# Kernel tuning notes

Hardware: AMD Instinct MI355X
Metric: run time of the kernel (lower is better)

Reference implementation:

```python
import jax, jax.numpy as jnp
import numpy as np

N = 20000      # nodes (spots)
D = 256        # embed_dim
H = 4          # n_heads
DH = D // H    # head dim
L = 2          # n_layers
E = 320000     # edges (avg degree 16)
K = 48         # static padded-neighbor cap (>= true max degree for this data)
EPS = 1e-5
NEG = -1e30


def setup_inputs() -> dict:
    key = jax.random.key(0)
    ks = jax.random.split(key, 8)
    s = 0.05
    return {
        "expr_embed": jax.random.normal(ks[0], (N, D), jnp.float32),
        "spatial_embed": jax.random.normal(ks[1], (N, D), jnp.float32),
        "in_proj_w": jax.random.normal(ks[2], (L, 3 * D, D), jnp.float32) * s,
        "in_proj_b": jnp.zeros((L, 3 * D), jnp.float32),
        "out_proj_w": jax.random.normal(ks[3], (L, D, D), jnp.float32) * s,
        "out_proj_b": jnp.zeros((L, D), jnp.float32),
        "ffn_w1": jax.random.normal(ks[4], (L, 2 * D, D), jnp.float32) * s,
        "ffn_b1": jnp.zeros((L, 2 * D), jnp.float32),
        "ffn_w2": jax.random.normal(ks[5], (L, D, 2 * D), jnp.float32) * s,
        "ffn_b2": jnp.zeros((L, D), jnp.float32),
        "ln1_g": jnp.ones((L, D), jnp.float32),
        "ln1_b": jnp.zeros((L, D), jnp.float32),
        "ln2_g": jnp.ones((L, D), jnp.float32),
        "ln2_b": jnp.zeros((L, D), jnp.float32),
        "edge_index": jax.random.randint(ks[6], (2, E), 0, N, jnp.int32),
    }


def _build_neighbors(edge_index):
    """Padded neighbor indices (N,K) and key_padding_mask (N,K) (True = pad)."""
    src, tgt = edge_index[0], edge_index[1]
    counts = jnp.zeros((N,), jnp.int32).at[tgt].add(1)
    order = jnp.argsort(tgt)                       # group edges by target
    src_s, tgt_s = src[order], tgt[order]
    offsets = jnp.concatenate([jnp.zeros((1,), jnp.int32),
                               jnp.cumsum(counts)[:-1].astype(jnp.int32)])
    pos = jnp.arange(E, dtype=jnp.int32) - offsets[tgt_s]
    pos = jnp.where(pos < K, pos, K)               # K is out-of-bounds -> dropped
    nbr = jnp.zeros((N, K), jnp.int32).at[tgt_s, pos].set(src_s, mode='drop')
    pad = jnp.ones((N, K), bool).at[tgt_s, pos].set(False, mode='drop')
    iso = counts == 0                              # isolated spots attend to self
    nbr = nbr.at[:, 0].set(jnp.where(iso, jnp.arange(N, dtype=jnp.int32), nbr[:, 0]))
    pad = pad.at[:, 0].set(jnp.where(iso, False, pad[:, 0]))
    return nbr, pad


def _layernorm(x, g, b):
    mu = jnp.mean(x, -1, keepdims=True)
    var = jnp.var(x, -1, keepdims=True)
    return (x - mu) * jax.lax.rsqrt(var + EPS) * g + b


def _forward(expr_embed, spatial_embed, in_proj_w, in_proj_b, out_proj_w,
             out_proj_b, ffn_w1, ffn_b1, ffn_w2, ffn_b2,
             ln1_g, ln1_b, ln2_g, ln2_b, nbr, pad):
    x = expr_embed
    scale = 1.0 / jnp.sqrt(jnp.asarray(DH, x.dtype))
    for i in range(L):
        Wq, Wk, Wv = jnp.split(in_proj_w[i], 3, axis=0)
        bq, bk, bv = jnp.split(in_proj_b[i], 3, axis=0)
        q = (x @ Wq.T + bq).reshape(N, H, DH)
        # project spatial once, gather projected rows (same math as gather-then-project)
        k = (spatial_embed @ Wk.T + bk)[nbr].reshape(N, K, H, DH)
        v = (spatial_embed @ Wv.T + bv)[nbr].reshape(N, K, H, DH)
        scores = jnp.einsum('nhd,nkhd->nhk', q, k) * scale      # (N,H,K)
        scores = jnp.where(pad[:, None, :], NEG, scores)
        attn = jax.nn.softmax(scores, axis=-1)
        ao = jnp.einsum('nhk,nkhd->nhd', attn, v).reshape(N, D)
        ao = ao @ out_proj_w[i].T + out_proj_b[i]
        x = _layernorm(x + ao, ln1_g[i], ln1_b[i])
        h = jax.nn.gelu(x @ ffn_w1[i].T + ffn_b1[i], approximate=False)
        h = h @ ffn_w2[i].T + ffn_b2[i]
        x = _layernorm(x + h, ln2_g[i], ln2_b[i])
    return x


def reference(expr_embed, spatial_embed, in_proj_w, in_proj_b, out_proj_w,
              out_proj_b, ffn_w1, ffn_b1, ffn_w2, ffn_b2,
              ln1_g, ln1_b, ln2_g, ln2_b, edge_index):
    nbr, pad = _build_neighbors(edge_index.astype(jnp.int32))
    return _forward(expr_embed, spatial_embed, in_proj_w, in_proj_b, out_proj_w,
                    out_proj_b, ffn_w1, ffn_b1, ffn_w2, ffn_b2,
                    ln1_g, ln1_b, ln2_g, ln2_b, nbr, pad)
```

## Files before the change

kernel.cpp:

```cpp
#include <hip/hip_runtime.h>

#define N_NODES 20000
#define DIM 256
#define NHEAD 4
#define DHEAD 64
#define NLAYER 2
#define NEDGE 320000
#define KCAP 48
#define NBM64 313
#define NBM32 625

typedef __bf16 v8bf __attribute__((ext_vector_type(8)));
typedef __bf16 v2bf __attribute__((ext_vector_type(2)));
typedef float v4f __attribute__((ext_vector_type(4)));

union U32 { unsigned u; v2bf v; };

__device__ __forceinline__ unsigned short f2bf(float f) {
    unsigned u = __float_as_uint(f);
    unsigned r = u + 0x7FFFu + ((u >> 16) & 1u);
    return (unsigned short)(r >> 16);
}
__device__ __forceinline__ float bflo(unsigned u) { return __uint_as_float(u << 16); }
__device__ __forceinline__ float bfhi(unsigned u) { return __uint_as_float(u & 0xFFFF0000u); }

__device__ __forceinline__ void gl2lds(const void* g, void* l) {
    __builtin_amdgcn_global_load_lds(
        (const __attribute__((address_space(1))) unsigned int*)g,
        (__attribute__((address_space(3))) unsigned int*)l, 16, 0, 0);
}

__device__ __forceinline__ void stage8(const unsigned short* __restrict__ g0,
                                       size_t stride_e, unsigned short* lds) {
    const int l = threadIdx.x & 63;
    const int r = l >> 3;
    const int c = (l & 7) ^ r;
    gl2lds(g0 + (size_t)r * stride_e + c * 8, lds);
}
__device__ __forceinline__ void stage8c(const unsigned short* __restrict__ base,
                                        int row0, int rowmax, size_t stride_e,
                                        int k0, unsigned short* lds) {
    const int l = threadIdx.x & 63;
    const int r = l >> 3;
    const int c = (l & 7) ^ r;
    int row = row0 + r; row = row > rowmax ? rowmax : row;
    gl2lds(base + (size_t)row * stride_e + k0 + c * 8, lds);
}

__device__ __forceinline__ v8bf frag_read(const unsigned short* lds, int row, int col2) {
    const int bo = row * 128 + (col2 ^ ((row & 7) << 4));
    return *(const v8bf*)((const char*)lds + bo);
}

__global__ void sniffzero_kernel(const unsigned short* __restrict__ p,
                                 int* __restrict__ flag, int* __restrict__ cnt) {
    if (blockIdx.x == 0) {
        __shared__ int s;
        if (threadIdx.x == 0) s = 0;
        __syncthreads();
        int c = 0;
        for (int i = threadIdx.x; i < 4096; i += 256) {
            unsigned short u = p[i];
            unsigned e = (u >> 7) & 0xFFu;
            if (e == 0xFFu) c++;
            else if (e == 0u && (u & 0x7Fu)) c++;
        }
        atomicAdd(&s, c);
        __syncthreads();
        if (threadIdx.x == 0) flag[0] = (s >= 4) ? 1 : 0;
    } else {
        int i = (blockIdx.x - 1) * 256 + threadIdx.x;
        if (i < N_NODES) cnt[i] = 0;
    }
}

struct ConvBfArgs { const void* src[6]; unsigned short* dst[6]; int n[6]; };

__global__ void conv_bf16_kernel(ConvBfArgs a, const int* __restrict__ flag) {
    const int t  = blockIdx.y;
    const int n  = a.n[t];
    const int i0 = (blockIdx.x * 256 + threadIdx.x) * 4;
    if (i0 >= n) return;
    unsigned short* dst = a.dst[t];
    if (flag[0]) {
        float4 v = *(const float4*)((const float*)a.src[t] + i0);
        ushort4 o;
        o.x = f2bf(v.x); o.y = f2bf(v.y); o.z = f2bf(v.z); o.w = f2bf(v.w);
        *(ushort4*)(dst + i0) = o;
    } else {
        ushort4 u = *(const ushort4*)((const unsigned short*)a.src[t] + i0);
        *(ushort4*)(dst + i0) = u;
    }
}

struct ConvF32Args { const void* src[8]; float* dst[8]; int n[8]; };

__global__ void conv_f32_kernel(ConvF32Args a, const int* __restrict__ flag) {
    const int t  = blockIdx.y;
    const int n  = a.n[t];
    const int i0 = (blockIdx.x * 256 + threadIdx.x) * 4;
    if (i0 >= n) return;
    float* dst = a.dst[t];
    if (flag[0]) {
        float4 v = *(const float4*)((const float*)a.src[t] + i0);
        *(float4*)(dst + i0) = v;
    } else {
        ushort4 u = *(const ushort4*)((const unsigned short*)a.src[t] + i0);
        *(float4*)(dst + i0) = make_float4(bflo(u.x), bflo(u.y), bflo(u.z), bflo(u.w));
    }
}

__global__ void build_nbr_kernel(const int* __restrict__ ei,
                                 int* __restrict__ cnt, int* __restrict__ nbr) {
    int e = blockIdx.x * 256 + threadIdx.x;
    if (e >= NEDGE) return;
    int s = ei[e];
    int t = ei[NEDGE + e];
    int slot = atomicAdd(&cnt[t], 1);
    if (slot < KCAP) nbr[t * KCAP + slot] = s;
}

__device__ __forceinline__ void gemm_body64(
    unsigned short* At, unsigned short* Bt,
    const unsigned short* __restrict__ A, const unsigned short* __restrict__ B,
    const float* __restrict__ bias, unsigned short* __restrict__ C,
    int M, int Nc, int Kd, int m0, int nB, int nC, int do_gelu)
{
    const int tid  = threadIdx.x;
    const int wave = tid >> 6;
    const int lane = tid & 63;
    const int wr   = (wave >> 1) * 32;
    const int wc   = (wave & 1) * 64;
    const int lm   = lane & 15;
    const int lk   = (lane >> 4) * 8;

    v4f acc[2][4] = {};

    for (int k0 = 0; k0 < Kd; k0 += 64) {
#pragma unroll
        for (int i = 0; i < 2; ++i) {
            const int rr = wave * 16 + i * 8;
            stage8c(A, m0 + rr, M - 1, Kd, k0, At + rr * 64);
        }
#pragma unroll
        for (int i = 0; i < 4; ++i) {
            const int rr = wave * 32 + i * 8;
            stage8(B + (size_t)(nB + rr) * Kd + k0, Kd, Bt + rr * 64);
        }
        __syncthreads();

#pragma unroll
        for (int ks = 0; ks < 2; ++ks) {
            v8bf af[2], bq[4];
#pragma unroll
            for (int mi = 0; mi < 2; ++mi)
                af[mi] = frag_read(At, wr + mi * 16 + lm, (ks * 32 + lk) * 2);
#pragma unroll
            for (int ni = 0; ni < 4; ++ni)
                bq[ni] = frag_read(Bt, wc + ni * 16 + lm, (ks * 32 + lk) * 2);
#pragma unroll
            for (int mi = 0; mi < 2; ++mi)
#pragma unroll
                for (int ni = 0; ni < 4; ++ni)
                    acc[mi][ni] = __builtin_amdgcn_mfma_f32_16x16x32_bf16(
                        af[mi], bq[ni], acc[mi][ni], 0, 0, 0);
        }
        __syncthreads();
    }

    const int rq = (lane >> 4) << 2;
#pragma unroll
    for (int ni = 0; ni < 4; ++ni) {
        int colb = wc + ni * 16 + lm;
        float bv = bias[nB + colb];
        int colc = nC + colb;
#pragma unroll
        for (int mi = 0; mi < 2; ++mi) {
#pragma unroll
            for (int r = 0; r < 4; ++r) {
                int row = m0 + wr + mi * 16 + rq + r;
                if (row >= M) continue;
                float v = acc[mi][ni][r] + bv;
                if (do_gelu) v = 0.5f * v * (1.0f + erff(v * 0.7071067811865475f));
                C[(size_t)row * Nc + colc] = f2bf(v);
            }
        }
    }
}

__global__ __launch_bounds__(256) void gemm_kernel(
    const unsigned short* __restrict__ A, const unsigned short* __restrict__ B,
    const float* __restrict__ bias, unsigned short* __restrict__ C,
    int M, int Nc, int Kd, int do_gelu)
{
    __shared__ __align__(1024) unsigned short At[64 * 64];
    __shared__ __align__(1024) unsigned short Bt[128 * 64];
    const int n0 = blockIdx.y * 128;
    gemm_body64(At, Bt, A, B, bias, C, M, Nc, Kd, blockIdx.x * 64, n0, n0, do_gelu);
}

__global__ __launch_bounds__(256) void qkv_kernel(
    const unsigned short* __restrict__ x, const unsigned short* __restrict__ spat,
    const unsigned short* __restrict__ W, const float* __restrict__ bias,
    unsigned short* __restrict__ q, unsigned short* __restrict__ kv, int M)
{
    __shared__ __align__(1024) unsigned short At[64 * 64];
    __shared__ __align__(1024) unsigned short Bt[128 * 64];
    const int y = blockIdx.y;
    const unsigned short* A = (y < 2) ? x : spat;
    unsigned short*       C = (y < 2) ? q : kv;
    const int Nc = (y < 2) ? 256 : 512;
    const int nB = y * 128;
    const int nC = (y < 2) ? nB : nB - 256;
    gemm_body64(At, Bt, A, W, bias, C, M, Nc, 256, blockIdx.x * 64, nB, nC, 0);
}

__global__ __launch_bounds__(256) void gemm_ln_kernel(
    const unsigned short* __restrict__ A, const unsigned short* __restrict__ B,
    const float* __restrict__ bias, const unsigned short* __restrict__ xres,
    const float* __restrict__ g, const float* __restrict__ bb,
    unsigned short* __restrict__ xout, void* __restrict__ dout,
    int M, int Kd, int final_out, const int* __restrict__ flag)
{
    __shared__ __align__(1024) unsigned short At[32 * 64];
    __shared__ __align__(1024) unsigned short Bt[256 * 64];
    __shared__ float partS[4][32], partSS[4][32];
    __shared__ float totMu[32], totR[32];

    const int tid  = threadIdx.x;
    const int m0   = blockIdx.x * 32;
    const int wave = tid >> 6;
    const int lane = tid & 63;
    const int wn0  = wave * 64;
    const int lm   = lane & 15;
    const int lk   = (lane >> 4) * 8;

    v4f acc[2][4] = {};

    for (int k0 = 0; k0 < Kd; k0 += 64) {
        {
            const int rr = wave * 8;
            stage8c(A, m0 + rr, M - 1, Kd, k0, At + rr * 64);
        }
#pragma unroll
        for (int i = 0; i < 8; ++i) {
            const int rr = wave * 64 + i * 8;
            stage8(B + (size_t)rr * Kd + k0, Kd, Bt + rr * 64);
        }
        __syncthreads();

#pragma unroll
        for (int ks = 0; ks < 2; ++ks) {
            v8bf af[2], bq[4];
#pragma unroll
            for (int mi = 0; mi < 2; ++mi)
                af[mi] = frag_read(At, mi * 16 + lm, (ks * 32 + lk) * 2);
#pragma unroll
            for (int ni = 0; ni < 4; ++ni)
                bq[ni] = frag_read(Bt, wn0 + ni * 16 + lm, (ks * 32 + lk) * 2);
#pragma unroll
            for (int mi = 0; mi < 2; ++mi)
#pragma unroll
                for (int ni = 0; ni < 4; ++ni)
                    acc[mi][ni] = __builtin_amdgcn_mfma_f32_16x16x32_bf16(
                        af[mi], bq[ni], acc[mi][ni], 0, 0, 0);
        }
        __syncthreads();
    }

    const int rq = (lane >> 4) << 2;
    float gv[4], bv2[4], biasv[4];
#pragma unroll
    for (int ni = 0; ni < 4; ++ni) {
        int col = wn0 + ni * 16 + lm;
        biasv[ni] = bias[col];
        gv[ni]    = g[col];
        bv2[ni]   = bb[col];
    }

    float sl[2][4] = {}, ssl[2][4] = {};
#pragma unroll
    for (int mi = 0; mi < 2; ++mi) {
#pragma unroll
        for (int r = 0; r < 4; ++r) {
            int row = m0 + mi * 16 + rq + r;
#pragma unroll
            for (int ni = 0; ni < 4; ++ni) {
                int col = wn0 + ni * 16 + lm;
                float resv = bflo((unsigned)xres[(size_t)row * DIM + col]);
                float v = acc[mi][ni][r] + biasv[ni] + resv;
                acc[mi][ni][r] = v;
                sl[mi][r]  += v;
                ssl[mi][r] += v * v;
            }
        }
    }
#pragma unroll
    for (int mi = 0; mi < 2; ++mi)
#pragma unroll
        for (int r = 0; r < 4; ++r) {
#pragma unroll
            for (int m = 1; m <= 8; m <<= 1) {
                sl[mi][r]  += __shfl_xor(sl[mi][r],  m, 64);
                ssl[mi][r] += __shfl_xor(ssl[mi][r], m, 64);
            }
        }
    if (lm == 0) {
#pragma unroll
        for (int mi = 0; mi < 2; ++mi)
#pragma unroll
            for (int r = 0; r < 4; ++r) {
                partS[wave][mi * 16 + rq + r]  = sl[mi][r];
                partSS[wave][mi * 16 + rq + r] = ssl[mi][r];
            }
    }
    __syncthreads();
    if (tid < 32) {
        float S = partS[0][tid] + partS[1][tid] + partS[2][tid] + partS[3][tid];
        float SS = partSS[0][tid] + partSS[1][tid] + partSS[2][tid] + partSS[3][tid];
        float mu  = S * (1.0f / DIM);
        float var = SS * (1.0f / DIM) - mu * mu;
        totMu[tid] = mu;
        totR[tid]  = rsqrtf(var + 1e-5f);
    }
    __syncthreads();

#pragma unroll
    for (int mi = 0; mi < 2; ++mi) {
#pragma unroll
        for (int r = 0; r < 4; ++r) {
            int lrow = mi * 16 + rq + r;
            int row  = m0 + lrow;
            float mu = totMu[lrow];
            float rv = totR[lrow];
#pragma unroll
            for (int ni = 0; ni < 4; ++ni) {
                int col = wn0 + ni * 16 + lm;
                float o = (acc[mi][ni][r] - mu) * rv * gv[ni] + bv2[ni];
                if (final_out) {
                    if (flag[0]) ((float*)dout)[(size_t)row * DIM + col] = o;
                    else ((unsigned short*)dout)[(size_t)row * DIM + col] = f2bf(o);
                } else {
                    xout[(size_t)row * DIM + col] = f2bf(o);
                }
            }
        }
    }
}

__global__ __launch_bounds__(256) void attn_kernel(
    const unsigned short* __restrict__ q,
    const unsigned short* __restrict__ kv,
    const int* __restrict__ nbr,
    const int* __restrict__ cnt,
    unsigned short* __restrict__ ao)
{
    const int n    = blockIdx.x;
    const int tid  = threadIdx.x;
    const int h    = tid >> 6;
    const int lane = tid & 63;

    __shared__ float sc[NHEAD][KCAP];
    __shared__ int   nbs[NHEAD][KCAP];

    int deg = cnt[n];
    if (deg > KCAP) deg = KCAP;
    const bool iso = (deg == 0);
    if (iso) deg = 1;

    if (lane < KCAP)
        nbs[h][lane] = (lane < deg) ? (iso ? n : nbr[n * KCAP + lane]) : 0;

    const int sub = lane & 7;
    const int grp = lane >> 3;
    const uint4 qu = *(const uint4*)&q[(size_t)n * DIM + h * DHEAD + sub * 8];
    const unsigned short* kbase = kv + h * DHEAD + sub * 8;
    const int nit = (deg + 7) >> 3;

    const int quarter = lane >> 4;
    const int d0      = (lane & 15) * 4;
    const unsigned short* vbase = kv + 256 + h * DHEAD + d0;
    const int dmax = (deg + 3) & ~3;
    const int npv  = dmax >> 2;

    uint4 ku[6];
#pragma unroll
    for (int it = 0; it < 6; ++it) {
        if (it < nit) {
            int nb = nbs[h][it * 8 + grp];
            ku[it] = *(const uint4*)&kbase[(size_t)nb * 512];
        }
    }
    uint2 vu[8];
#pragma unroll
    for (int it = 0; it < 8; ++it) {
        if (it < npv) {
            int nb = nbs[h][it * 4 + quarter];
            vu[it] = *(const uint2*)&vbase[(size_t)nb * 512];
        }
    }

#pragma unroll
    for (int it = 0; it < 6; ++it) {
        if (it < nit) {
            int j = it * 8 + grp;
            uint4 kz = ku[it];
#if __has_builtin(__builtin_amdgcn_fdot2_f32_bf16)
            U32 a0{qu.x}, a1{qu.y}, a2{qu.z}, a3{qu.w};
            U32 b0{kz.x}, b1{kz.y}, b2{kz.z}, b3{kz.w};
            float p = __builtin_amdgcn_fdot2_f32_bf16(a0.v, b0.v, 0.0f, false);
            p = __builtin_amdgcn_fdot2_f32_bf16(a1.v, b1.v, p, false);
            p = __builtin_amdgcn_fdot2_f32_bf16(a2.v, b2.v, p, false);
            p = __builtin_amdgcn_fdot2_f32_bf16(a3.v, b3.v, p, false);
#else
            float p = bflo(qu.x) * bflo(kz.x);
            p = fmaf(bfhi(qu.x), bfhi(kz.x), p);
            p = fmaf(bflo(qu.y), bflo(kz.y), p);
            p = fmaf(bfhi(qu.y), bfhi(kz.y), p);
            p = fmaf(bflo(qu.z), bflo(kz.z), p);
            p = fmaf(bfhi(qu.z), bfhi(kz.z), p);
            p = fmaf(bflo(qu.w), bflo(kz.w), p);
            p = fmaf(bfhi(qu.w), bfhi(kz.w), p);
#endif
            p += __shfl_xor(p, 1, 64);
            p += __shfl_xor(p, 2, 64);
            p += __shfl_xor(p, 4, 64);
            if (sub == 0 && j < deg) sc[h][j] = p * 0.125f;
        }
    }

    {
        float s  = (lane < deg) ? sc[h][lane] : -1e30f;
        float mx = s;
#pragma unroll
        for (int m = 32; m >= 1; m >>= 1) mx = fmaxf(mx, __shfl_xor(mx, m, 64));
        float e   = (lane < deg) ? __expf(s - mx) : 0.0f;
        float sum = e;
#pragma unroll
        for (int m = 32; m >= 1; m >>= 1) sum += __shfl_xor(sum, m, 64);
        float inv = 1.0f / sum;
        if (lane < KCAP) sc[h][lane] = e * inv;
    }

    {
        float a0 = 0.f, a1 = 0.f, a2 = 0.f, a3 = 0.f;
#pragma unroll
        for (int it = 0; it < 8; ++it) {
            if (it < npv) {
                float w = sc[h][it * 4 + quarter];
                uint2 u = vu[it];
                a0 = fmaf(w, bflo(u.x), a0);
                a1 = fmaf(w, bfhi(u.x), a1);
                a2 = fmaf(w, bflo(u.y), a2);
                a3 = fmaf(w, bfhi(u.y), a3);
            }
        }
        for (int j = 32; j < dmax; j += 4) {
            int j0 = j + quarter;
            int nb = nbs[h][j0];
            uint2 u = *(const uint2*)&vbase[(size_t)nb * 512];
            float w = sc[h][j0];
            a0 = fmaf(w, bflo(u.x), a0);
            a1 = fmaf(w, bfhi(u.x), a1);
            a2 = fmaf(w, bflo(u.y), a2);
            a3 = fmaf(w, bfhi(u.y), a3);
        }
        a0 += __shfl_xor(a0, 16, 64); a0 += __shfl_xor(a0, 32, 64);
        a1 += __shfl_xor(a1, 16, 64); a1 += __shfl_xor(a1, 32, 64);
        a2 += __shfl_xor(a2, 16, 64); a2 += __shfl_xor(a2, 32, 64);
        a3 += __shfl_xor(a3, 16, 64); a3 += __shfl_xor(a3, 32, 64);
        if (lane < 16) {
            uint2 o;
            o.x = (unsigned)f2bf(a0) | ((unsigned)f2bf(a1) << 16);
            o.y = (unsigned)f2bf(a2) | ((unsigned)f2bf(a3) << 16);
            *(uint2*)&ao[(size_t)n * DIM + h * DHEAD + d0] = o;
        }
    }
}

extern "C" void kernel_launch(void* const* d_in, const int* in_sizes, int n_in,
                              void* d_out, int out_size, void* d_ws, size_t ws_size,
                              hipStream_t stream) {
    const int* ei = (const int*)d_in[14];

    char* ws = (char*)d_ws;
    size_t off = 0;
    auto alloc = [&](size_t bytes) -> void* {
        void* p = ws + off;
        off = (off + bytes + 255) & ~(size_t)255;
        return p;
    };

    const int bidx[6] = { 0, 1, 2, 4, 6, 8 };
    const int bnn[6]  = { N_NODES * DIM, N_NODES * DIM,
                          NLAYER * 3 * DIM * DIM, NLAYER * DIM * DIM,
                          NLAYER * 2 * DIM * DIM, NLAYER * DIM * 2 * DIM };
    ConvBfArgs cb;
    unsigned short* canb[6];
    for (int i = 0; i < 6; ++i) {
        canb[i] = (unsigned short*)alloc((size_t)bnn[i] * 2);
        cb.src[i] = d_in[bidx[i]];
        cb.dst[i] = canb[i];
        cb.n[i]   = bnn[i];
    }
    const unsigned short* expr_b = canb[0];
    const unsigned short* spat_b = canb[1];
    const unsigned short* ipw    = canb[2];
    const unsigned short* opw    = canb[3];
    const unsigned short* w1     = canb[4];
    const unsigned short* w2     = canb[5];

    const int fidx[8] = { 3, 5, 7, 9, 10, 11, 12, 13 };
    const int fn[8]   = { NLAYER * 3 * DIM, NLAYER * DIM, NLAYER * 2 * DIM,
                          NLAYER * DIM, NLAYER * DIM, NLAYER * DIM,
                          NLAYER * DIM, NLAYER * DIM };
    ConvF32Args cf;
    float* canf[8];
    for (int i = 0; i < 8; ++i) {
        canf[i] = (float*)alloc((size_t)fn[i] * 4);
        cf.src[i] = d_in[fidx[i]];
        cf.dst[i] = canf[i];
        cf.n[i]   = fn[i];
    }

    unsigned short* x_buf  = (unsigned short*)alloc((size_t)N_NODES * DIM * 2);
    unsigned short* q_buf  = (unsigned short*)alloc((size_t)N_NODES * DIM * 2);
    unsigned short* kv_buf = (unsigned short*)alloc((size_t)N_NODES * 2 * DIM * 2);
    unsigned short* ao_buf = (unsigned short*)alloc((size_t)N_NODES * DIM * 2);
    unsigned short* h_buf  = (unsigned short*)alloc((size_t)N_NODES * 2 * DIM * 2);
    int* cnt  = (int*)alloc((size_t)N_NODES * 4);
    int* nbr  = (int*)alloc((size_t)N_NODES * KCAP * 4);
    int* flag = (int*)alloc(256);

    sniffzero_kernel<<<1 + (N_NODES + 255) / 256, 256, 0, stream>>>(
        (const unsigned short*)d_in[0], flag, cnt);
    conv_bf16_kernel<<<dim3((N_NODES * DIM) / 1024, 6), 256, 0, stream>>>(cb, flag);
    conv_f32_kernel<<<dim3(2, 8), 256, 0, stream>>>(cf, flag);
    build_nbr_kernel<<<(NEDGE + 255) / 256, 256, 0, stream>>>(ei, cnt, nbr);

    for (int i = 0; i < NLAYER; ++i) {
        const unsigned short* Wqkv = ipw + (size_t)i * 3 * DIM * DIM;
        const float*          bqkv = canf[0] + (size_t)i * 3 * DIM;
        const unsigned short* xin  = (i == 0) ? expr_b : x_buf;

        qkv_kernel<<<dim3(NBM64, 6), 256, 0, stream>>>(
            xin, spat_b, Wqkv, bqkv, q_buf, kv_buf, N_NODES);
        attn_kernel<<<N_NODES, 256, 0, stream>>>(q_buf, kv_buf, nbr, cnt, ao_buf);
        gemm_ln_kernel<<<NBM32, 256, 0, stream>>>(
            ao_buf, opw + (size_t)i * DIM * DIM, canf[1] + (size_t)i * DIM,
            xin, canf[4] + (size_t)i * DIM, canf[5] + (size_t)i * DIM,
            x_buf, nullptr, N_NODES, DIM, 0, flag);
        gemm_kernel<<<dim3(NBM64, 4), 256, 0, stream>>>(
            x_buf, w1 + (size_t)i * 2 * DIM * DIM, canf[2] + (size_t)i * 2 * DIM,
            h_buf, N_NODES, 2 * DIM, DIM, 1);
        gemm_ln_kernel<<<NBM32, 256, 0, stream>>>(
            h_buf, w2 + (size_t)i * DIM * 2 * DIM, canf[3] + (size_t)i * DIM,
            x_buf, canf[6] + (size_t)i * DIM, canf[7] + (size_t)i * DIM,
            x_buf, d_out, N_NODES, 2 * DIM, (i == NLAYER - 1) ? 1 : 0, flag);
    }
}
```

Measured before the change: 399.4 us.

## Fuse FFN up-projection, GELU, down-projection and LayerNorm into one kernel

Replaces the separate W1 GEMM (with GELU) and the W2 GEMM+LayerNorm kernels with a single kernel per 32-row tile. The tile streams W1/W2 in 32-column chunks, keeps the GELU hidden activations in LDS, and accumulates the second GEMM in registers before the residual add and LayerNorm. This removes the global round trip of the N×512 hidden buffer and one launch per layer. In exchange, every block re-reads the full W1 and W2 through cache, uses small per-wave MFMA tiles, and needs three barriers per chunk, so the kernel may become latency-bound.

```diff
diff --git a/kernel.cpp b/kernel.cpp
--- a/kernel.cpp
+++ b/kernel.cpp
@@ -49,6 +49,11 @@
 
 __device__ __forceinline__ v8bf frag_read(const unsigned short* lds, int row, int col2) {
     const int bo = row * 128 + (col2 ^ ((row & 7) << 4));
+    return *(const v8bf*)((const char*)lds + bo);
+}
+
+__device__ __forceinline__ v8bf frag32(const unsigned short* lds, int row, int t) {
+    const int bo = row * 64 + (((t ^ ((row >> 1) & 3))) << 4);
     return *(const v8bf*)((const char*)lds + bo);
 }
 
@@ -124,7 +129,7 @@
     unsigned short* At, unsigned short* Bt,
     const unsigned short* __restrict__ A, const unsigned short* __restrict__ B,
     const float* __restrict__ bias, unsigned short* __restrict__ C,
-    int M, int Nc, int Kd, int m0, int nB, int nC, int do_gelu)
+    int M, int Nc, int Kd, int m0, int nB, int nC)
 {
     const int tid  = threadIdx.x;
     const int wave = tid >> 6;
@@ -181,22 +186,10 @@
                 int row = m0 + wr + mi * 16 + rq + r;
                 if (row >= M) continue;
                 float v = acc[mi][ni][r] + bv;
-                if (do_gelu) v = 0.5f * v * (1.0f + erff(v * 0.7071067811865475f));
                 C[(size_t)row * Nc + colc] = f2bf(v);
             }
         }
     }
-}
-
-__global__ __launch_bounds__(256) void gemm_kernel(
-    const unsigned short* __restrict__ A, const unsigned short* __restrict__ B,
-    const float* __restrict__ bias, unsigned short* __restrict__ C,
-    int M, int Nc, int Kd, int do_gelu)
-{
-    __shared__ __align__(1024) unsigned short At[64 * 64];
-    __shared__ __align__(1024) unsigned short Bt[128 * 64];
-    const int n0 = blockIdx.y * 128;
-    gemm_body64(At, Bt, A, B, bias, C, M, Nc, Kd, blockIdx.x * 64, n0, n0, do_gelu);
 }
 
 __global__ __launch_bounds__(256) void qkv_kernel(
@@ -212,15 +205,14 @@
     const int Nc = (y < 2) ? 256 : 512;
     const int nB = y * 128;
     const int nC = (y < 2) ? nB : nB - 256;
-    gemm_body64(At, Bt, A, W, bias, C, M, Nc, 256, blockIdx.x * 64, nB, nC, 0);
+    gemm_body64(At, Bt, A, W, bias, C, M, Nc, 256, blockIdx.x * 64, nB, nC);
 }
 
 __global__ __launch_bounds__(256) void gemm_ln_kernel(
     const unsigned short* __restrict__ A, const unsigned short* __restrict__ B,
     const float* __restrict__ bias, const unsigned short* __restrict__ xres,
     const float* __restrict__ g, const float* __restrict__ bb,
-    unsigned short* __restrict__ xout, void* __restrict__ dout,
-    int M, int Kd, int final_out, const int* __restrict__ flag)
+    unsigned short* __restrict__ xout, int M, int Kd)
 {
     __shared__ __align__(1024) unsigned short At[32 * 64];
     __shared__ __align__(1024) unsigned short Bt[256 * 64];
@@ -337,6 +329,195 @@
             for (int ni = 0; ni < 4; ++ni) {
                 int col = wn0 + ni * 16 + lm;
                 float o = (acc[mi][ni][r] - mu) * rv * gv[ni] + bv2[ni];
+                xout[(size_t)row * DIM + col] = f2bf(o);
+            }
+        }
+    }
+}
+
+__global__ __launch_bounds__(256) void ffn_fused_kernel(
+    const unsigned short* __restrict__ x,
+    const unsigned short* __restrict__ W1,
+    const float* __restrict__ b1,
+    const unsigned short* __restrict__ W2,
+    const float* __restrict__ b2,
+    const float* __restrict__ g, const float* __restrict__ bb,
+    unsigned short* __restrict__ xout, void* __restrict__ dout,
+    int final_out, const int* __restrict__ flag)
+{
+    __shared__ __align__(1024) unsigned short Xt[4 * 32 * 64];
+    __shared__ __align__(1024) unsigned short W1t[32 * 256];
+    __shared__ __align__(1024) unsigned short W2t[256 * 32];
+    __shared__ __align__(1024) unsigned short Ht[32 * 32];
+    __shared__ float partS[4][32], partSS[4][32];
+    __shared__ float totMu[32], totR[32];
+
+    const int tid  = threadIdx.x;
+    const int wave = tid >> 6;
+    const int lane = tid & 63;
+    const int m0   = blockIdx.x * 32;
+    const int lm   = lane & 15;
+    const int lk   = (lane >> 4) * 8;
+    const int lt   = lane >> 4;
+    const int rq   = (lane >> 4) << 2;
+
+    const int r1    = tid >> 3;
+    const int cbase = (tid & 7) * 4;
+    uint4 w1r[4], w2r[4];
+    auto LOADW = [&](int j) {
+#pragma unroll
+        for (int i = 0; i < 4; ++i)
+            w1r[i] = *(const uint4*)&W1[(size_t)(j * 32 + r1) * 256 + (cbase + i) * 8];
+#pragma unroll
+        for (int i = 0; i < 4; ++i)
+            w2r[i] = *(const uint4*)&W2[(size_t)tid * 512 + j * 32 + i * 8];
+    };
+    auto WRITEW = [&]() {
+#pragma unroll
+        for (int i = 0; i < 4; ++i) {
+            int byo = r1 * 512 + (((cbase + i) * 16) ^ ((r1 & 7) << 4));
+            *(uint4*)((char*)W1t + byo) = w1r[i];
+        }
+#pragma unroll
+        for (int i = 0; i < 4; ++i) {
+            int byo = tid * 64 + ((i * 16) ^ (((tid >> 1) & 3) << 4));
+            *(uint4*)((char*)W2t + byo) = w2r[i];
+        }
+    };
+
+    LOADW(0);
+#pragma unroll
+    for (int i = 0; i < 4; ++i)
+        stage8(x + (size_t)(m0 + i * 8) * 256 + wave * 64, 256,
+               Xt + wave * 2048 + i * 8 * 64);
+    __syncthreads();
+
+    v8bf af1[8];
+    const int arow = (wave >> 1) * 16 + lm;
+#pragma unroll
+    for (int c = 0; c < 4; ++c)
+#pragma unroll
+        for (int ks = 0; ks < 2; ++ks)
+            af1[c * 2 + ks] = frag_read(Xt + c * 2048, arow, (ks * 32 + lk) * 2);
+
+    v4f acc2[2][4] = {};
+    const int brow1 = (wave & 1) * 16 + lm;
+    const int hcol  = (wave & 1) * 16 + lm;
+    const int hrow0 = (wave >> 1) * 16 + rq;
+
+    for (int j = 0; j < 16; ++j) {
+        WRITEW();
+        __syncthreads();
+        if (j + 1 < 16) LOADW(j + 1);
+
+        v4f a1 = {0.f, 0.f, 0.f, 0.f};
+#pragma unroll
+        for (int kk = 0; kk < 8; ++kk) {
+            v8bf bq = *(const v8bf*)((const char*)W1t +
+                        brow1 * 512 + ((kk * 64 + lt * 16) ^ ((brow1 & 7) << 4)));
+            a1 = __builtin_amdgcn_mfma_f32_16x16x32_bf16(af1[kk], bq, a1, 0, 0, 0);
+        }
+        {
+            float b1v = b1[j * 32 + hcol];
+#pragma unroll
+            for (int r = 0; r < 4; ++r) {
+                float v = a1[r] + b1v;
+                v = 0.5f * v * (1.0f + erff(v * 0.7071067811865475f));
+                int row = hrow0 + r;
+                int byo = row * 64 + ((hcol * 2) ^ (((row >> 1) & 3) << 4));
+                *(unsigned short*)((char*)Ht + byo) = f2bf(v);
+            }
+        }
+        __syncthreads();
+
+        {
+            v8bf af2[2];
+#pragma unroll
+            for (int mi = 0; mi < 2; ++mi)
+                af2[mi] = frag32(Ht, mi * 16 + lm, lt);
+#pragma unroll
+            for (int ni = 0; ni < 4; ++ni) {
+                v8bf bq2 = frag32(W2t, wave * 64 + ni * 16 + lm, lt);
+                acc2[0][ni] = __builtin_amdgcn_mfma_f32_16x16x32_bf16(
+                    af2[0], bq2, acc2[0][ni], 0, 0, 0);
+                acc2[1][ni] = __builtin_amdgcn_mfma_f32_16x16x32_bf16(
+                    af2[1], bq2, acc2[1][ni], 0, 0, 0);
+            }
+        }
+        __syncthreads();
+    }
+
+    const int wn0 = wave * 64;
+    float gv[4], bv2[4], biasv[4];
+#pragma unroll
+    for (int ni = 0; ni < 4; ++ni) {
+        int col = wn0 + ni * 16 + lm;
+        biasv[ni] = b2[col];
+        gv[ni]    = g[col];
+        bv2[ni]   = bb[col];
+    }
+
+    float sl[2][4] = {}, ssl[2][4] = {};
+#pragma unroll
+    for (int mi = 0; mi < 2; ++mi) {
+#pragma unroll
+        for (int r = 0; r < 4; ++r) {
+            int row = mi * 16 + rq + r;
+#pragma unroll
+            for (int ni = 0; ni < 4; ++ni) {
+                int coll = ni * 16 + lm;
+                int byo = row * 128 + ((coll * 2) ^ ((row & 7) << 4));
+                float resv = bflo(*(const unsigned short*)
+                                  ((const char*)(Xt + wave * 2048) + byo));
+                float v = acc2[mi][ni][r] + biasv[ni] + resv;
+                acc2[mi][ni][r] = v;
+                sl[mi][r]  += v;
+                ssl[mi][r] += v * v;
+            }
+        }
+    }
+#pragma unroll
+    for (int mi = 0; mi < 2; ++mi)
+#pragma unroll
+        for (int r = 0; r < 4; ++r) {
+#pragma unroll
+            for (int m = 1; m <= 8; m <<= 1) {
+                sl[mi][r]  += __shfl_xor(sl[mi][r],  m, 64);
+                ssl[mi][r] += __shfl_xor(ssl[mi][r], m, 64);
+            }
+        }
+    if (lm == 0) {
+#pragma unroll
+        for (int mi = 0; mi < 2; ++mi)
+#pragma unroll
+            for (int r = 0; r < 4; ++r) {
+                partS[wave][mi * 16 + rq + r]  = sl[mi][r];
+                partSS[wave][mi * 16 + rq + r] = ssl[mi][r];
+            }
+    }
+    __syncthreads();
+    if (tid < 32) {
+        float S = partS[0][tid] + partS[1][tid] + partS[2][tid] + partS[3][tid];
+        float SS = partSS[0][tid] + partSS[1][tid] + partSS[2][tid] + partSS[3][tid];
+        float mu  = S * (1.0f / DIM);
+        float var = SS * (1.0f / DIM) - mu * mu;
+        totMu[tid] = mu;
+        totR[tid]  = rsqrtf(var + 1e-5f);
+    }
+    __syncthreads();
+
+#pragma unroll
+    for (int mi = 0; mi < 2; ++mi) {
+#pragma unroll
+        for (int r = 0; r < 4; ++r) {
+            int lrow = mi * 16 + rq + r;
+            int row  = m0 + lrow;
+            float mu = totMu[lrow];
+            float rv = totR[lrow];
+#pragma unroll
+            for (int ni = 0; ni < 4; ++ni) {
+                int col = wn0 + ni * 16 + lm;
+                float o = (acc2[mi][ni][r] - mu) * rv * gv[ni] + bv2[ni];
                 if (final_out) {
                     if (flag[0]) ((float*)dout)[(size_t)row * DIM + col] = o;
                     else ((unsigned short*)dout)[(size_t)row * DIM + col] = f2bf(o);
@@ -527,7 +708,6 @@
     unsigned short* q_buf  = (unsigned short*)alloc((size_t)N_NODES * DIM * 2);
     unsigned short* kv_buf = (unsigned short*)alloc((size_t)N_NODES * 2 * DIM * 2);
     unsigned short* ao_buf = (unsigned short*)alloc((size_t)N_NODES * DIM * 2);
-    unsigned short* h_buf  = (unsigned short*)alloc((size_t)N_NODES * 2 * DIM * 2);
     int* cnt  = (int*)alloc((size_t)N_NODES * 4);
     int* nbr  = (int*)alloc((size_t)N_NODES * KCAP * 4);
     int* flag = (int*)alloc(256);
@@ -549,13 +729,11 @@
         gemm_ln_kernel<<<NBM32, 256, 0, stream>>>(
             ao_buf, opw + (size_t)i * DIM * DIM, canf[1] + (size_t)i * DIM,
             xin, canf[4] + (size_t)i * DIM, canf[5] + (size_t)i * DIM,
-            x_buf, nullptr, N_NODES, DIM, 0, flag);
-        gemm_kernel<<<dim3(NBM64, 4), 256, 0, stream>>>(
+            x_buf, N_NODES, DIM);
+        ffn_fused_kernel<<<NBM32, 256, 0, stream>>>(
             x_buf, w1 + (size_t)i * 2 * DIM * DIM, canf[2] + (size_t)i * 2 * DIM,
-            h_buf, N_NODES, 2 * DIM, DIM, 1);
-        gemm_ln_kernel<<<NBM32, 256, 0, stream>>>(
-            h_buf, w2 + (size_t)i * DIM * 2 * DIM, canf[3] + (size_t)i * DIM,
-            x_buf, canf[6] + (size_t)i * DIM, canf[7] + (size_t)i * DIM,
-            x_buf, d_out, N_NODES, 2 * DIM, (i == NLAYER - 1) ? 1 : 0, flag);
-    }
-}
+            w2 + (size_t)i * DIM * 2 * DIM, canf[3] + (size_t)i * DIM,
+            canf[6] + (size_t)i * DIM, canf[7] + (size_t)i * DIM,
+            x_buf, d_out, (i == NLAYER - 1) ? 1 : 0, flag);
+    }
+}
```

Result: slower. 570.1 us (+42.7%).
